# Kernel tuning notes

Hardware: AMD Instinct MI355X
Metric: run time of the kernel (lower is better)

Reference implementation:

```python
import jax, jax.numpy as jnp
import numpy as np

N = 2048
TEMP = 1.0


def _conv(x, w, b):
    y = jax.lax.conv_general_dilated(x, w, (1, 1), 'VALID',
                                     dimension_numbers=('NCHW', 'OIHW', 'NCHW'))
    return y + b[None, :, None, None]


def _pool(x):
    return jax.lax.reduce_window(x, -jnp.inf, jax.lax.max,
                                 (1, 1, 2, 2), (1, 1, 2, 2), 'VALID')


def setup_inputs() -> dict:
    key = jax.random.key(0)
    ks = jax.random.split(key, 20)
    s = 0.05
    idx = jnp.arange(N)
    positions = jnp.stack([idx // 64, idx % 64], axis=1).astype(jnp.int32)  # 32x64 grid
    return {
        'x': jax.random.normal(ks[0], (1, N, 1, 32, 32), jnp.float32),
        'positions': positions,
        'conv1_w': jax.random.normal(ks[1], (36, 1, 4, 4), jnp.float32) * s,
        'conv1_b': jnp.zeros((36,), jnp.float32),
        'conv2_w': jax.random.normal(ks[2], (48, 36, 3, 3), jnp.float32) * s,
        'conv2_b': jnp.zeros((48,), jnp.float32),
        'fc1_w': jax.random.normal(ks[3], (512, 1728), jnp.float32) * s,
        'fc1_b': jnp.zeros((512,), jnp.float32),
        'fc2_w': jax.random.normal(ks[4], (512, 512), jnp.float32) * s,
        'fc2_b': jnp.zeros((512,), jnp.float32),
        'nbr_w': jax.random.normal(ks[5], (512, 512), jnp.float32) * s,
        'nbr_b': jnp.zeros((512,), jnp.float32),
        'templates': jax.random.normal(ks[6], (10, 1024), jnp.float32),
        'proto_w': jax.random.normal(ks[7], (1024, 1024), jnp.float32) * s,
        'proto_b': jnp.zeros((1024,), jnp.float32),
        'glob_w1': jax.random.normal(ks[8], (128, 1024), jnp.float32) * s,
        'glob_b1': jnp.zeros((128,), jnp.float32),
        'glob_w2': jax.random.normal(ks[9], (1, 128), jnp.float32) * s,
        'glob_b2': jnp.zeros((1,), jnp.float32),
        'cls_w': jax.random.normal(ks[10], (2, 1024), jnp.float32) * s,
        'cls_b': jnp.zeros((2,), jnp.float32),
    }


def reference(x, positions, conv1_w, conv1_b, conv2_w, conv2_b,
              fc1_w, fc1_b, fc2_w, fc2_b, nbr_w, nbr_b,
              templates, proto_w, proto_b, glob_w1, glob_b1,
              glob_w2, glob_b2, cls_w, cls_b):
    xs = x[0]                                    # squeeze bag dim -> [N,1,32,32]
    h = _pool(jax.nn.relu(_conv(xs, conv1_w, conv1_b)))
    h = _pool(jax.nn.relu(_conv(h, conv2_w, conv2_b)))
    H = h.reshape(h.shape[0], -1)                # [N,1728]
    H = jax.nn.relu(H @ fc1_w.T + fc1_b)         # dropout is identity in eval
    H = jax.nn.relu(H @ fc2_w.T + fc2_b)         # [N,512]

    # --- neighbourhood attention (vectorized GAT-style gather/softmax) ---
    d = jnp.max(jnp.abs(positions[:, None, :] - positions[None, :, :]), axis=-1)
    mask = (d > 0) & (d <= 1)                    # [N,N] neighbor mask
    has = mask.any(axis=1)
    mask = jnp.where(has[:, None], mask, jnp.eye(mask.shape[0], dtype=bool))  # fallback: self
    An = jnp.tanh(H @ nbr_w.T + nbr_b)           # [N,512]
    logits = H @ An.T                            # logits[i,j] = tanh(W h_j) . h_i
    alphas = jax.nn.softmax(jnp.where(mask, logits, -jnp.inf), axis=1)
    Hn = alphas @ H                              # neighbourhood embeddings [N,512]
    H2 = jnp.concatenate([H, Hn], axis=1)        # [N,1024]

    # --- template (prototype) attention ---
    betas = jax.nn.softmax((jnp.tanh(H2 @ proto_w.T + proto_b) @ templates.T).T / TEMP, axis=1)  # [T,N]
    embs = betas @ H2                            # [T,1024]

    # --- global attention over templates ---
    g = jnp.tanh(embs @ glob_w1.T + glob_b1) @ glob_w2.T + glob_b2  # [T,1]
    gammas = jax.nn.softmax(g.T / TEMP, axis=1)  # [1,T]
    M = gammas @ embs                            # [1,1024]
    A = gammas @ betas                           # [1,N]
    Y_prob = jax.nn.sigmoid(M @ cls_w.T + cls_b) # [1,2]
    Y_hat = jnp.argmax(Y_prob, axis=1)
    return Y_prob, Y_hat, A
```

## Files before the change

### kernel.cpp

```cpp
#include <hip/hip_runtime.h>
#include <hip/hip_bf16.h>
#include <math.h>


typedef short short8 __attribute__((ext_vector_type(8)));
typedef float f32x4  __attribute__((ext_vector_type(4)));

__device__ inline short f2bf(float f) {
    unsigned u = __builtin_bit_cast(unsigned, f);
    u += 0x7fff + ((u >> 16) & 1);
    return (short)(u >> 16);
}
__device__ inline float bf2f(short h) {
    unsigned u = ((unsigned)(unsigned short)h) << 16;
    return __builtin_bit_cast(float, u);
}
__device__ inline f32x4 mfma16(short8 a, short8 b, f32x4 c) {
    return __builtin_amdgcn_mfma_f32_16x16x32_bf16(a, b, c, 0, 0, 0);
}
__device__ inline void splitstore(const float* s, short* hi, short* lo, int i) {
    float f = s[i];
    short h = f2bf(f);
    hi[i] = h;
    lo[i] = f2bf(f - bf2f(h));
}

__global__ __launch_bounds__(256) void prep_all_kernel(
    const float* __restrict__ fc1w, short* __restrict__ fc1whi, short* __restrict__ fc1wlo,
    const float* __restrict__ fc2w, short* __restrict__ fc2whi, short* __restrict__ fc2wlo,
    const float* __restrict__ nbrw, short* __restrict__ nbrwhi, short* __restrict__ nbrwlo,
    const float* __restrict__ prw,  short* __restrict__ prwhi,  short* __restrict__ prwlo,
    const float* __restrict__ w1,   short* __restrict__ w1m,
    const float* __restrict__ w2,   short* __restrict__ w2m,
    float* __restrict__ St, float* __restrict__ embs)
{
    const int b = blockIdx.x, tid = threadIdx.x;
    if (b < 3456) {
        int i = b*256 + tid; if (i < 884736) splitstore(fc1w, fc1whi, fc1wlo, i);
    } else if (b < 4480) {
        int i = (b-3456)*256 + tid; if (i < 262144) splitstore(fc2w, fc2whi, fc2wlo, i);
    } else if (b < 5504) {
        int i = (b-4480)*256 + tid; if (i < 262144) splitstore(nbrw, nbrwhi, nbrwlo, i);
    } else if (b < 9600) {
        int i = (b-5504)*256 + tid; if (i < 1048576) splitstore(prw, prwhi, prwlo, i);
    } else if (b < 9606) {
        int i = (b-9600)*256 + tid;
        if (i < 1536) {
            int c = i >> 5, k = i & 31;
            w1m[i] = (c < 36 && k < 16) ? f2bf(w1[c*16 + k]) : (short)0;
        }
    } else if (b < 9714) {
        int i = (b-9606)*256 + tid;
        if (i < 27648) {
            int oc = i / 576, r = i % 576, tap = r >> 6, c = r & 63;
            w2m[i] = (c < 36) ? f2bf(w2[oc*324 + c*9 + tap]) : (short)0;
        }
    } else if (b < 9794) {
        int i = (b-9714)*256 + tid; if (i < 20480) St[i] = 0.0f;
    } else {
        int i = (b-9794)*256 + tid; if (i < 10240) embs[i] = 0.0f;
    }
}

__global__ __launch_bounds__(64, 2) void conv_mfma_kernel(
    const float* __restrict__ x,
    const short* __restrict__ w1m,
    const float* __restrict__ b1,
    const short* __restrict__ w2m,
    const float* __restrict__ b2,
    short* __restrict__ Hfhi)
{
    __shared__ __align__(16) short sxb[2][1024];
    __shared__ __align__(16) short sh1[196*40 + 32];
    const int n = blockIdx.x, l = threadIdx.x;
    const int g = l >> 4, fr = l & 15;

    #pragma unroll
    for (int i = 0; i < 4; ++i) {
        const float4 v4 = ((const float4*)(x + (size_t)n*1024))[l + 64*i];
        short v[4] = { f2bf(v4.x), f2bf(v4.y), f2bf(v4.z), f2bf(v4.w) };
        const int c4 = (l + 64*i)*4;
        *(short4*)&sxb[0][c4] = *(short4*)v;
        if (c4 & 31) sxb[1][c4-1] = v[0];
        sxb[1][c4+0] = v[1];
        sxb[1][c4+1] = v[2];
        sxb[1][c4+2] = v[3];
    }
    if (l < 4) { short8 z = {}; *(short8*)&sh1[196*40 + l*8] = z; }
    short8 bw1[3];
    #pragma unroll
    for (int nt = 0; nt < 3; ++nt)
        bw1[nt] = *(const short8*)(w1m + (nt*16 + fr)*32 + g*8);
    __syncthreads();

    for (int mt = 0; mt < 49; ++mt) {
        const int pp = mt*16 + fr;
        const int q = pp >> 2, dd = pp & 3;
        const int iy0 = 2*(q/14) + (dd >> 1), ix0 = 2*(q%14) + (dd & 1);
        short8 af = {};
        if (g < 2) {
            const int par = ix0 & 1;
            const int colp = ix0 - par;
            const unsigned* p0 = (const unsigned*)&sxb[par][(iy0 + 2*g)*32 + colp];
            union { unsigned u[4]; short8 s; } uu;
            uu.u[0] = p0[0];  uu.u[1] = p0[1];
            uu.u[2] = p0[16]; uu.u[3] = p0[17];
            af = uu.s;
        }
        f32x4 acc[3] = {};
        #pragma unroll
        for (int nt = 0; nt < 3; ++nt) acc[nt] = mfma16(af, bw1[nt], acc[nt]);
        const int q1 = mt*4 + g;
        #pragma unroll
        for (int nt = 0; nt < 3; ++nt) {
            const int c = nt*16 + fr;
            if (c < 36) {
                float m = fmaxf(fmaxf(acc[nt][0], acc[nt][1]),
                                fmaxf(acc[nt][2], acc[nt][3]));
                m = fmaxf(m + b1[c], 0.0f);
                *(short*)((char*)sh1 + (q1*80 + c*2)) = f2bf(m);
            } else if (c < 40) {
                *(short*)((char*)sh1 + (q1*80 + c*2)) = 0;
            }
        }
    }
    __syncthreads();

    #pragma unroll
    for (int nt = 0; nt < 3; ++nt) {
        short8 bfr[18];
        {
            const short* wb = w2m + (size_t)(nt*16 + fr)*576 + g*8;
            #pragma unroll
            for (int ks = 0; ks < 18; ++ks)
                bfr[ks] = *(const short8*)(wb + ks*32);
        }
        for (int mt = 0; mt < 9; ++mt) {
            const int pp = mt*16 + fr;
            const int q2 = pp >> 2, dd = pp & 3;
            const int oy = 2*(q2/6) + (dd >> 1), ox = 2*(q2%6) + (dd & 1);
            f32x4 acc = {};
            #pragma unroll
            for (int ks = 0; ks < 18; ++ks) {
                const int tap = ks >> 1, half = ks & 1;
                const int hr = (oy + tap/3)*14 + ox + tap%3;
                const short8 a = *(const short8*)((char*)sh1 +
                    (hr*80 + half*64 + g*16));
                acc = mfma16(a, bfr[ks], acc);
            }
            const int oc = nt*16 + fr;
            float m = fmaxf(fmaxf(acc[0], acc[1]), fmaxf(acc[2], acc[3]));
            m = fmaxf(m + b2[oc], 0.0f);
            Hfhi[(size_t)n*1728 + oc*36 + (mt*4 + g)] = f2bf(m);
        }
    }
}

template<int ACT, int OUTF32, int OUTBF, int TSC>
__global__ __launch_bounds__(256) void gemm_split_kernel(
    const short* __restrict__ Ahi,
    const short* __restrict__ Whi, const short* __restrict__ Wlo,
    const float* __restrict__ bias,
    float* __restrict__ Cf, short* __restrict__ Chi,
    const float* __restrict__ Tm, float* __restrict__ St,
    const int N, const int K)
{
    __shared__ __align__(16) short sA[4096];
    __shared__ __align__(16) short sB[2][4096];
    const int bn = blockIdx.x, bm = blockIdx.y;
    const int tid = threadIdx.x, l = tid & 63, w = tid >> 6, g = l >> 4, fr = l & 15;
    const int srow = tid >> 2, kc = (tid & 3) << 4;
    const size_t aoff = (size_t)(bm*64 + srow)*K + kc;
    const size_t boff = (size_t)(bn*64 + srow)*K + kc;
    const int swb = (srow & 7) << 4;
    const int wbase = srow*128 + kc*2;
    f32x4 acc[4] = {};
    for (int k0 = 0; k0 < K; k0 += 64) {
        const short8 a0 = *(const short8*)(Ahi + aoff + k0);
        const short8 a1 = *(const short8*)(Ahi + aoff + k0 + 8);
        const short8 b0 = *(const short8*)(Whi + boff + k0);
        const short8 b1 = *(const short8*)(Whi + boff + k0 + 8);
        const short8 b2 = *(const short8*)(Wlo + boff + k0);
        const short8 b3 = *(const short8*)(Wlo + boff + k0 + 8);
        __syncthreads();
        *(short8*)((char*)&sA[0]    + ((wbase     ) ^ swb)) = a0;
        *(short8*)((char*)&sA[0]    + ((wbase + 16) ^ swb)) = a1;
        *(short8*)((char*)&sB[0][0] + ((wbase     ) ^ swb)) = b0;
        *(short8*)((char*)&sB[0][0] + ((wbase + 16) ^ swb)) = b1;
        *(short8*)((char*)&sB[1][0] + ((wbase     ) ^ swb)) = b2;
        *(short8*)((char*)&sB[1][0] + ((wbase + 16) ^ swb)) = b3;
        __syncthreads();
        const int ar = w*16 + fr, asw = (ar & 7) << 4;
        const short8 ah0 = *(const short8*)((char*)&sA[0] + ((ar*128      + g*16) ^ asw));
        const short8 ah1 = *(const short8*)((char*)&sA[0] + ((ar*128 + 64 + g*16) ^ asw));
        #pragma unroll
        for (int nt = 0; nt < 4; ++nt) {
            const int br = nt*16 + fr, bsw = (br & 7) << 4;
            const short8 bh0 = *(const short8*)((char*)&sB[0][0] + ((br*128      + g*16) ^ bsw));
            const short8 bh1 = *(const short8*)((char*)&sB[0][0] + ((br*128 + 64 + g*16) ^ bsw));
            const short8 bl0 = *(const short8*)((char*)&sB[1][0] + ((br*128      + g*16) ^ bsw));
            const short8 bl1 = *(const short8*)((char*)&sB[1][0] + ((br*128 + 64 + g*16) ^ bsw));
            acc[nt] = mfma16(ah0, bh0, acc[nt]);
            acc[nt] = mfma16(ah1, bh1, acc[nt]);
            acc[nt] = mfma16(ah0, bl0, acc[nt]);
            acc[nt] = mfma16(ah1, bl1, acc[nt]);
        }
    }
    float pv[4][4];
    #pragma unroll
    for (int nt = 0; nt < 4; ++nt) {
        const int col = bn*64 + nt*16 + fr;
        const float bv = bias[col];
        #pragma unroll
        for (int i = 0; i < 4; ++i) {
            const int row = bm*64 + w*16 + g*4 + i;
            float v = acc[nt][i] + bv;
            if (ACT == 1) v = fmaxf(v, 0.0f);
            if (ACT == 2) v = tanhf(v);
            pv[nt][i] = v;
            const size_t idx = (size_t)row*N + col;
            if (OUTF32) Cf[idx] = v;
            if (OUTBF)  Chi[idx] = f2bf(v);
        }
    }
    if (TSC) {
        for (int t = 0; t < 10; ++t) {
            float tm[4];
            #pragma unroll
            for (int nt = 0; nt < 4; ++nt)
                tm[nt] = Tm[t*1024 + bn*64 + nt*16 + fr];
            float part[4];
            #pragma unroll
            for (int i = 0; i < 4; ++i) {
                float s = 0.0f;
                #pragma unroll
                for (int nt = 0; nt < 4; ++nt) s = fmaf(pv[nt][i], tm[nt], s);
                #pragma unroll
                for (int m = 1; m <= 8; m <<= 1) s += __shfl_xor(s, m);
                part[i] = s;
            }
            if (fr == 0) {
                #pragma unroll
                for (int i = 0; i < 4; ++i)
                    atomicAdd(&St[t*2048 + bm*64 + w*16 + g*4 + i], part[i]);
            }
        }
    }
}

__global__ __launch_bounds__(64) void nbr_attn_kernel(
    const float* __restrict__ H, const float* __restrict__ An,
    short* __restrict__ H2hi)
{
    const int i = blockIdx.x;
    const int lane = threadIdx.x;
    const int r = i >> 6, c = i & 63;
    const int DR[8] = {-1,-1,-1, 0, 0, 1, 1, 1};
    const int DC[8] = {-1, 0, 1,-1, 1,-1, 0, 1};
    int nbr[8]; bool val[8];
    #pragma unroll
    for (int j = 0; j < 8; ++j) {
        const int rr = r + DR[j], cc = c + DC[j];
        val[j] = (rr >= 0 && rr < 32 && cc >= 0 && cc < 64);
        nbr[j] = val[j] ? rr*64 + cc : i;
    }
    float hi[8];
    #pragma unroll
    for (int q = 0; q < 8; ++q) hi[q] = H[(size_t)i*512 + q*64 + lane];
    float av[8][8];
    #pragma unroll
    for (int j = 0; j < 8; ++j) {
        const float* an = An + (size_t)nbr[j]*512 + lane;
        #pragma unroll
        for (int q = 0; q < 8; ++q) av[j][q] = an[q*64];
    }
    float lg[8];
    #pragma unroll
    for (int j = 0; j < 8; ++j) {
        float s = 0.0f;
        #pragma unroll
        for (int q = 0; q < 8; ++q) s = fmaf(hi[q], av[j][q], s);
        #pragma unroll
        for (int off = 32; off; off >>= 1) s += __shfl_xor(s, off);
        lg[j] = val[j] ? s : -1e30f;
    }
    float mx = -1e30f;
    #pragma unroll
    for (int j = 0; j < 8; ++j) mx = fmaxf(mx, lg[j]);
    float sum = 0.0f; float al[8];
    #pragma unroll
    for (int j = 0; j < 8; ++j) { al[j] = expf(lg[j]-mx); sum += al[j]; }
    const float inv = 1.0f/sum;
    #pragma unroll
    for (int j = 0; j < 8; ++j) {
        const float* hj = H + (size_t)nbr[j]*512 + lane;
        #pragma unroll
        for (int q = 0; q < 8; ++q) av[j][q] = hj[q*64];
    }
    float hn[8] = {};
    #pragma unroll
    for (int j = 0; j < 8; ++j) {
        const float a = al[j]*inv;
        #pragma unroll
        for (int q = 0; q < 8; ++q) hn[q] = fmaf(a, av[j][q], hn[q]);
    }
    #pragma unroll
    for (int q = 0; q < 8; ++q) {
        const size_t i0 = (size_t)i*1024 + q*64 + lane;
        H2hi[i0]       = f2bf(hi[q]);
        H2hi[i0 + 512] = f2bf(hn[q]);
    }
}

__global__ __launch_bounds__(256) void beta_embs_kernel(
    const float* __restrict__ St,
    const short* __restrict__ H2hi,
    float* __restrict__ embs,
    float* __restrict__ minv)
{
    const int t = blockIdx.y;
    const int tid = threadIdx.x;
    __shared__ float red[256];
    __shared__ float sb[256];
    float mx = -1e30f;
    for (int n = tid; n < 2048; n += 256) mx = fmaxf(mx, St[t*2048+n]);
    red[tid] = mx; __syncthreads();
    for (int s = 128; s; s >>= 1) { if (tid < s) red[tid] = fmaxf(red[tid], red[tid+s]); __syncthreads(); }
    mx = red[0]; __syncthreads();
    float sum = 0.0f;
    for (int n = tid; n < 2048; n += 256) sum += expf(St[t*2048+n]-mx);
    red[tid] = sum; __syncthreads();
    for (int s = 128; s; s >>= 1) { if (tid < s) red[tid] += red[tid+s]; __syncthreads(); }
    const float inv = 1.0f/red[0];
    if (blockIdx.x == 0 && tid == 0) { minv[t*2+0] = mx; minv[t*2+1] = inv; }
    const int colc = blockIdx.x & 3;
    const int nc   = blockIdx.x >> 2;
    sb[tid] = expf(St[t*2048 + nc*256 + tid] - mx) * inv;
    __syncthreads();
    const int col = colc*256 + tid;
    float acc = 0.0f;
    for (int j = 0; j < 256; ++j)
        acc = fmaf(sb[j], bf2f(H2hi[(size_t)(nc*256+j)*1024 + col]), acc);
    atomicAdd(&embs[t*1024+col], acc);
}

__global__ __launch_bounds__(64) void glob_g2_kernel(
    const float* __restrict__ embs, const float* __restrict__ gw1,
    const float* __restrict__ gb1, const float* __restrict__ gw2,
    float* __restrict__ gpart)
{
    const int k = blockIdx.x, t = blockIdx.y, lane = threadIdx.x;
    const float* e  = embs + t*1024 + lane;
    const float* wv = gw1 + k*1024 + lane;
    float s = 0.0f;
    #pragma unroll
    for (int q = 0; q < 16; ++q) s = fmaf(e[q*64], wv[q*64], s);
    #pragma unroll
    for (int off = 32; off; off >>= 1) s += __shfl_xor(s, off);
    if (lane == 0) gpart[t*128 + k] = tanhf(s + gb1[k]) * gw2[k];
}

__global__ __launch_bounds__(256) void final3_kernel(
    const float* __restrict__ gpart, const float* __restrict__ gb2,
    const float* __restrict__ embs,  const float* __restrict__ St,
    const float* __restrict__ minv,
    const float* __restrict__ cw, const float* __restrict__ cb,
    float* __restrict__ out)
{
    __shared__ float gam[10];
    __shared__ float sM[1024];
    __shared__ float red[256];
    __shared__ float gv[10];
    __shared__ float smx[10], sinv[10];
    __shared__ float v0s;
    const int tid = threadIdx.x;
    for (int t = 0; t < 10; ++t) {
        float s = (tid < 128) ? gpart[t*128 + tid] : 0.0f;
        red[tid] = s; __syncthreads();
        for (int st = 128; st; st >>= 1) { if (tid < st) red[tid] += red[tid+st]; __syncthreads(); }
        if (tid == 0) gv[t] = red[0];
        __syncthreads();
    }
    if (tid < 10) { smx[tid] = minv[tid*2]; sinv[tid] = minv[tid*2+1]; }
    if (tid == 0) {
        float mx = -1e30f;
        for (int t = 0; t < 10; ++t) mx = fmaxf(mx, gv[t] + gb2[0]);
        float sum = 0.0f;
        for (int t = 0; t < 10; ++t) { gam[t] = expf(gv[t] + gb2[0] - mx); sum += gam[t]; }
        for (int t = 0; t < 10; ++t) gam[t] /= sum;
    }
    __syncthreads();
    for (int col = tid; col < 1024; col += 256) {
        float m = 0.0f;
        for (int t = 0; t < 10; ++t) m = fmaf(gam[t], embs[t*1024+col], m);
        sM[col] = m;
    }
    for (int n = tid; n < 2048; n += 256) {
        float a = 0.0f;
        for (int t = 0; t < 10; ++t)
            a = fmaf(gam[t], expf(St[t*2048+n]-smx[t])*sinv[t], a);
        out[3+n] = a;
    }
    __syncthreads();
    float s0 = 0.0f, s1 = 0.0f;
    for (int q = tid; q < 1024; q += 256) {
        s0 = fmaf(sM[q], cw[q], s0);
        s1 = fmaf(sM[q], cw[1024+q], s1);
    }
    red[tid] = s0; __syncthreads();
    for (int s = 128; s; s >>= 1) { if (tid < s) red[tid] += red[tid+s]; __syncthreads(); }
    if (tid == 0) v0s = red[0];
    __syncthreads();
    red[tid] = s1; __syncthreads();
    for (int s = 128; s; s >>= 1) { if (tid < s) red[tid] += red[tid+s]; __syncthreads(); }
    if (tid == 0) {
        const float l0 = v0s + cb[0], l1 = red[0] + cb[1];
        const float p0 = 1.0f/(1.0f+expf(-l0));
        const float p1 = 1.0f/(1.0f+expf(-l1));
        out[0] = p0; out[1] = p1;
        out[2] = (p1 > p0) ? 1.0f : 0.0f;
    }
}

extern "C" void kernel_launch(void* const* d_in, const int* in_sizes, int n_in,
                              void* d_out, int out_size, void* d_ws, size_t ws_size,
                              hipStream_t stream)
{
    (void)in_sizes; (void)n_in; (void)out_size; (void)ws_size;
    const float* x        = (const float*)d_in[0];
    const float* conv1_w  = (const float*)d_in[2];
    const float* conv1_b  = (const float*)d_in[3];
    const float* conv2_w  = (const float*)d_in[4];
    const float* conv2_b  = (const float*)d_in[5];
    const float* fc1_w    = (const float*)d_in[6];
    const float* fc1_b    = (const float*)d_in[7];
    const float* fc2_w    = (const float*)d_in[8];
    const float* fc2_b    = (const float*)d_in[9];
    const float* nbr_w    = (const float*)d_in[10];
    const float* nbr_b    = (const float*)d_in[11];
    const float* templ    = (const float*)d_in[12];
    const float* proto_w  = (const float*)d_in[13];
    const float* proto_b  = (const float*)d_in[14];
    const float* glob_w1  = (const float*)d_in[15];
    const float* glob_b1  = (const float*)d_in[16];
    const float* glob_w2  = (const float*)d_in[17];
    const float* glob_b2  = (const float*)d_in[18];
    const float* cls_w    = (const float*)d_in[19];
    const float* cls_b    = (const float*)d_in[20];
    float* out = (float*)d_out;

    char* p = (char*)d_ws;
    auto alloc = [&](size_t bytes) { char* r = p; p += (bytes + 255) & ~(size_t)255; return r; };
    short* Hfhi   = (short*)alloc((size_t)2048*1728*2);
    short* Hfc1hi = (short*)alloc((size_t)2048*512*2);
    float* H      = (float*)alloc((size_t)2048*512*4);
    short* Hhi    = (short*)alloc((size_t)2048*512*2);
    float* An     = (float*)alloc((size_t)2048*512*4);
    short* H2hi   = (short*)alloc((size_t)2048*1024*2);
    float* St     = (float*)alloc((size_t)10*2048*4);
    float* minv   = (float*)alloc(10*2*4);
    float* embs   = (float*)alloc((size_t)10*1024*4);
    float* gpart  = (float*)alloc((size_t)10*128*4);
    short* w1m    = (short*)alloc(1536*2);
    short* w2m    = (short*)alloc(27648*2);
    short* fc1whi = (short*)alloc((size_t)512*1728*2);
    short* fc1wlo = (short*)alloc((size_t)512*1728*2);
    short* fc2whi = (short*)alloc((size_t)512*512*2);
    short* fc2wlo = (short*)alloc((size_t)512*512*2);
    short* nbrwhi = (short*)alloc((size_t)512*512*2);
    short* nbrwlo = (short*)alloc((size_t)512*512*2);
    short* prwhi  = (short*)alloc((size_t)1024*1024*2);
    short* prwlo  = (short*)alloc((size_t)1024*1024*2);

    prep_all_kernel<<<9834, 256, 0, stream>>>(
        fc1_w, fc1whi, fc1wlo, fc2_w, fc2whi, fc2wlo,
        nbr_w, nbrwhi, nbrwlo, proto_w, prwhi, prwlo,
        conv1_w, w1m, conv2_w, w2m, St, embs);

    conv_mfma_kernel<<<2048, 64, 0, stream>>>(x, w1m, conv1_b, w2m, conv2_b, Hfhi);
    gemm_split_kernel<1,0,1,0><<<dim3(8,32), 256, 0, stream>>>(
        Hfhi, fc1whi, fc1wlo, fc1_b, nullptr, Hfc1hi, nullptr, nullptr, 512, 1728);
    gemm_split_kernel<1,1,1,0><<<dim3(8,32), 256, 0, stream>>>(
        Hfc1hi, fc2whi, fc2wlo, fc2_b, H, Hhi, nullptr, nullptr, 512, 512);
    gemm_split_kernel<2,1,0,0><<<dim3(8,32), 256, 0, stream>>>(
        Hhi, nbrwhi, nbrwlo, nbr_b, An, nullptr, nullptr, nullptr, 512, 512);
    nbr_attn_kernel<<<2048, 64, 0, stream>>>(H, An, H2hi);
    gemm_split_kernel<2,0,0,1><<<dim3(16,32), 256, 0, stream>>>(
        H2hi, prwhi, prwlo, proto_b, nullptr, nullptr, templ, St, 1024, 1024);
    beta_embs_kernel<<<dim3(32,10), 256, 0, stream>>>(St, H2hi, embs, minv);
    glob_g2_kernel<<<dim3(128,10), 64, 0, stream>>>(embs, glob_w1, glob_b1, glob_w2, gpart);
    final3_kernel<<<1, 256, 0, stream>>>(gpart, glob_b2, embs, St, minv, cls_w, cls_b, out);
}
```

Baseline: 167.5 us.

## Swizzle conv1 LDS layout and split GEMM tiles across eight waves with prefetch

In the conv kernel, the pooled conv1 output is stored in shared memory with a per-row rotation of its 16-byte chunks (modulo 5). The intent is to reduce LDS bank conflicts when conv2 reads from it. The split-bf16 GEMM now runs 512 threads per block, with 8 waves in a 4x2 arrangement, each owning two 16-column tiles instead of four. It also prefetches the next K-slice from global memory into registers while the current slice is computed. The goal is more waves and latency hiding per tile, at the cost of fewer accumulators per wave and more threads sharing each barrier.

New measurement: 179.8 us. 7.4% more time.

```diff
diff --git a/kernel.cpp b/kernel.cpp
--- a/kernel.cpp
+++ b/kernel.cpp
@@ -111,16 +111,20 @@
         #pragma unroll
         for (int nt = 0; nt < 3; ++nt) acc[nt] = mfma16(af, bw1[nt], acc[nt]);
         const int q1 = mt*4 + g;
+        const int q1m = q1 % 5;
         #pragma unroll
         for (int nt = 0; nt < 3; ++nt) {
             const int c = nt*16 + fr;
-            if (c < 36) {
-                float m = fmaxf(fmaxf(acc[nt][0], acc[nt][1]),
-                                fmaxf(acc[nt][2], acc[nt][3]));
-                m = fmaxf(m + b1[c], 0.0f);
-                *(short*)((char*)sh1 + (q1*80 + c*2)) = f2bf(m);
-            } else if (c < 40) {
-                *(short*)((char*)sh1 + (q1*80 + c*2)) = 0;
+            if (c < 40) {
+                short val = 0;
+                if (c < 36) {
+                    float m = fmaxf(fmaxf(acc[nt][0], acc[nt][1]),
+                                    fmaxf(acc[nt][2], acc[nt][3]));
+                    m = fmaxf(m + b1[c], 0.0f);
+                    val = f2bf(m);
+                }
+                int bb = (c >> 3) + q1m; if (bb >= 5) bb -= 5;
+                *(short*)((char*)sh1 + (q1*80 + bb*16 + (c & 7)*2)) = val;
             }
         }
     }
@@ -141,12 +145,14 @@
             const int oy = 2*(q2/6) + (dd >> 1), ox = 2*(q2%6) + (dd & 1);
             f32x4 acc = {};
             #pragma unroll
-            for (int ks = 0; ks < 18; ++ks) {
-                const int tap = ks >> 1, half = ks & 1;
+            for (int tap = 0; tap < 9; ++tap) {
                 const int hr = (oy + tap/3)*14 + ox + tap%3;
-                const short8 a = *(const short8*)((char*)sh1 +
-                    (hr*80 + half*64 + g*16));
-                acc = mfma16(a, bfr[ks], acc);
+                const int hm = hr % 5;
+                int b0 = g + hm;      if (b0 >= 5) b0 -= 5;
+                int b1i = 4 + g + hm; if (b1i >= 5) b1i -= 5; if (b1i >= 5) b1i -= 5;
+                const char* rb = (const char*)sh1 + hr*80;
+                acc = mfma16(*(const short8*)(rb + b0*16),  bfr[tap*2+0], acc);
+                acc = mfma16(*(const short8*)(rb + b1i*16), bfr[tap*2+1], acc);
             }
             const int oc = nt*16 + fr;
             float m = fmaxf(fmaxf(acc[0], acc[1]), fmaxf(acc[2], acc[3]));
@@ -157,7 +163,7 @@
 }
 
 template<int ACT, int OUTF32, int OUTBF, int TSC>
-__global__ __launch_bounds__(256) void gemm_split_kernel(
+__global__ __launch_bounds__(512, 2) void gemm_split_kernel(
     const short* __restrict__ Ahi,
     const short* __restrict__ Whi, const short* __restrict__ Wlo,
     const float* __restrict__ bias,
@@ -169,55 +175,55 @@
     __shared__ __align__(16) short sB[2][4096];
     const int bn = blockIdx.x, bm = blockIdx.y;
     const int tid = threadIdx.x, l = tid & 63, w = tid >> 6, g = l >> 4, fr = l & 15;
-    const int srow = tid >> 2, kc = (tid & 3) << 4;
-    const size_t aoff = (size_t)(bm*64 + srow)*K + kc;
-    const size_t boff = (size_t)(bn*64 + srow)*K + kc;
+    const int wm = w & 3, wn = w >> 2;
+    const int srow = tid >> 3;
+    const int wbyte = srow*128 + (tid & 7)*16;
     const int swb = (srow & 7) << 4;
-    const int wbase = srow*128 + kc*2;
-    f32x4 acc[4] = {};
+    const size_t aoff = (size_t)(bm*64 + srow)*K + (tid & 7)*8;
+    const size_t boff = (size_t)(bn*64 + srow)*K + (tid & 7)*8;
+    f32x4 acc[2] = {};
+    short8 ra = *(const short8*)(Ahi + aoff);
+    short8 rb0 = *(const short8*)(Whi + boff);
+    short8 rb1 = *(const short8*)(Wlo + boff);
     for (int k0 = 0; k0 < K; k0 += 64) {
-        const short8 a0 = *(const short8*)(Ahi + aoff + k0);
-        const short8 a1 = *(const short8*)(Ahi + aoff + k0 + 8);
-        const short8 b0 = *(const short8*)(Whi + boff + k0);
-        const short8 b1 = *(const short8*)(Whi + boff + k0 + 8);
-        const short8 b2 = *(const short8*)(Wlo + boff + k0);
-        const short8 b3 = *(const short8*)(Wlo + boff + k0 + 8);
         __syncthreads();
-        *(short8*)((char*)&sA[0]    + ((wbase     ) ^ swb)) = a0;
-        *(short8*)((char*)&sA[0]    + ((wbase + 16) ^ swb)) = a1;
-        *(short8*)((char*)&sB[0][0] + ((wbase     ) ^ swb)) = b0;
-        *(short8*)((char*)&sB[0][0] + ((wbase + 16) ^ swb)) = b1;
-        *(short8*)((char*)&sB[1][0] + ((wbase     ) ^ swb)) = b2;
-        *(short8*)((char*)&sB[1][0] + ((wbase + 16) ^ swb)) = b3;
+        *(short8*)((char*)sA       + (wbyte ^ swb)) = ra;
+        *(short8*)((char*)&sB[0][0] + (wbyte ^ swb)) = rb0;
+        *(short8*)((char*)&sB[1][0] + (wbyte ^ swb)) = rb1;
         __syncthreads();
-        const int ar = w*16 + fr, asw = (ar & 7) << 4;
-        const short8 ah0 = *(const short8*)((char*)&sA[0] + ((ar*128      + g*16) ^ asw));
-        const short8 ah1 = *(const short8*)((char*)&sA[0] + ((ar*128 + 64 + g*16) ^ asw));
-        #pragma unroll
-        for (int nt = 0; nt < 4; ++nt) {
-            const int br = nt*16 + fr, bsw = (br & 7) << 4;
+        if (k0 + 64 < K) {
+            ra  = *(const short8*)(Ahi + aoff + k0 + 64);
+            rb0 = *(const short8*)(Whi + boff + k0 + 64);
+            rb1 = *(const short8*)(Wlo + boff + k0 + 64);
+        }
+        const int ar = wm*16 + fr, asw = (ar & 7) << 4;
+        const short8 ah0 = *(const short8*)((char*)sA + ((ar*128      + g*16) ^ asw));
+        const short8 ah1 = *(const short8*)((char*)sA + ((ar*128 + 64 + g*16) ^ asw));
+        #pragma unroll
+        for (int ntl = 0; ntl < 2; ++ntl) {
+            const int br = (wn*2 + ntl)*16 + fr, bsw = (br & 7) << 4;
             const short8 bh0 = *(const short8*)((char*)&sB[0][0] + ((br*128      + g*16) ^ bsw));
             const short8 bh1 = *(const short8*)((char*)&sB[0][0] + ((br*128 + 64 + g*16) ^ bsw));
             const short8 bl0 = *(const short8*)((char*)&sB[1][0] + ((br*128      + g*16) ^ bsw));
             const short8 bl1 = *(const short8*)((char*)&sB[1][0] + ((br*128 + 64 + g*16) ^ bsw));
-            acc[nt] = mfma16(ah0, bh0, acc[nt]);
-            acc[nt] = mfma16(ah1, bh1, acc[nt]);
-            acc[nt] = mfma16(ah0, bl0, acc[nt]);
-            acc[nt] = mfma16(ah1, bl1, acc[nt]);
-        }
-    }
-    float pv[4][4];
-    #pragma unroll
-    for (int nt = 0; nt < 4; ++nt) {
-        const int col = bn*64 + nt*16 + fr;
+            acc[ntl] = mfma16(ah0, bh0, acc[ntl]);
+            acc[ntl] = mfma16(ah1, bh1, acc[ntl]);
+            acc[ntl] = mfma16(ah0, bl0, acc[ntl]);
+            acc[ntl] = mfma16(ah1, bl1, acc[ntl]);
+        }
+    }
+    float pv[2][4];
+    #pragma unroll
+    for (int ntl = 0; ntl < 2; ++ntl) {
+        const int col = bn*64 + (wn*2 + ntl)*16 + fr;
         const float bv = bias[col];
         #pragma unroll
         for (int i = 0; i < 4; ++i) {
-            const int row = bm*64 + w*16 + g*4 + i;
-            float v = acc[nt][i] + bv;
+            const int row = bm*64 + wm*16 + g*4 + i;
+            float v = acc[ntl][i] + bv;
             if (ACT == 1) v = fmaxf(v, 0.0f);
             if (ACT == 2) v = tanhf(v);
-            pv[nt][i] = v;
+            pv[ntl][i] = v;
             const size_t idx = (size_t)row*N + col;
             if (OUTF32) Cf[idx] = v;
             if (OUTBF)  Chi[idx] = f2bf(v);
@@ -225,16 +231,16 @@
     }
     if (TSC) {
         for (int t = 0; t < 10; ++t) {
-            float tm[4];
+            float tm[2];
             #pragma unroll
-            for (int nt = 0; nt < 4; ++nt)
-                tm[nt] = Tm[t*1024 + bn*64 + nt*16 + fr];
+            for (int ntl = 0; ntl < 2; ++ntl)
+                tm[ntl] = Tm[t*1024 + bn*64 + (wn*2 + ntl)*16 + fr];
             float part[4];
             #pragma unroll
             for (int i = 0; i < 4; ++i) {
                 float s = 0.0f;
                 #pragma unroll
-                for (int nt = 0; nt < 4; ++nt) s = fmaf(pv[nt][i], tm[nt], s);
+                for (int ntl = 0; ntl < 2; ++ntl) s = fmaf(pv[ntl][i], tm[ntl], s);
                 #pragma unroll
                 for (int m = 1; m <= 8; m <<= 1) s += __shfl_xor(s, m);
                 part[i] = s;
@@ -242,7 +248,7 @@
             if (fr == 0) {
                 #pragma unroll
                 for (int i = 0; i < 4; ++i)
-                    atomicAdd(&St[t*2048 + bm*64 + w*16 + g*4 + i], part[i]);
+                    atomicAdd(&St[t*2048 + bm*64 + wm*16 + g*4 + i], part[i]);
             }
         }
     }
@@ -478,14 +484,14 @@
         conv1_w, w1m, conv2_w, w2m, St, embs);
 
     conv_mfma_kernel<<<2048, 64, 0, stream>>>(x, w1m, conv1_b, w2m, conv2_b, Hfhi);
-    gemm_split_kernel<1,0,1,0><<<dim3(8,32), 256, 0, stream>>>(
+    gemm_split_kernel<1,0,1,0><<<dim3(8,32), 512, 0, stream>>>(
         Hfhi, fc1whi, fc1wlo, fc1_b, nullptr, Hfc1hi, nullptr, nullptr, 512, 1728);
-    gemm_split_kernel<1,1,1,0><<<dim3(8,32), 256, 0, stream>>>(
+    gemm_split_kernel<1,1,1,0><<<dim3(8,32), 512, 0, stream>>>(
         Hfc1hi, fc2whi, fc2wlo, fc2_b, H, Hhi, nullptr, nullptr, 512, 512);
-    gemm_split_kernel<2,1,0,0><<<dim3(8,32), 256, 0, stream>>>(
+    gemm_split_kernel<2,1,0,0><<<dim3(8,32), 512, 0, stream>>>(
         Hhi, nbrwhi, nbrwlo, nbr_b, An, nullptr, nullptr, nullptr, 512, 512);
     nbr_attn_kernel<<<2048, 64, 0, stream>>>(H, An, H2hi);
-    gemm_split_kernel<2,0,0,1><<<dim3(16,32), 256, 0, stream>>>(
+    gemm_split_kernel<2,0,0,1><<<dim3(16,32), 512, 0, stream>>>(
         H2hi, prwhi, prwlo, proto_b, nullptr, nullptr, templ, St, 1024, 1024);
     beta_embs_kernel<<<dim3(32,10), 256, 0, stream>>>(St, H2hi, embs, minv);
     glob_g2_kernel<<<dim3(128,10), 64, 0, stream>>>(embs, glob_w1, glob_b1, glob_w2, gpart);
```
